# Kernel optimization log

Measured on AMD Instinct MI355X. Metric: run time of the kernel, lower is better.

## Reference

```python
import jax, jax.numpy as jnp
import numpy as np

N_NODES = 200000
N_GRAPHS = 64
K_SLOTS = 16
LATENT = 128
HID = 128  # hidden_dim // 2


def setup_inputs() -> dict:
    key = jax.random.key(0)
    ks = jax.random.split(key, 8)
    z = jax.random.normal(ks[0], (N_GRAPHS, K_SLOTS, LATENT), dtype=jnp.float32)
    s = jax.random.uniform(ks[1], (N_NODES, K_SLOTS), dtype=jnp.float32)
    batch = jnp.sort(jax.random.randint(ks[2], (N_NODES,), 0, N_GRAPHS))
    sc1 = 1.0 / np.sqrt(LATENT)
    sc2 = 1.0 / np.sqrt(HID)
    W1 = jax.random.normal(ks[3], (LATENT, HID), dtype=jnp.float32) * sc1
    b1 = jnp.zeros((HID,), dtype=jnp.float32)
    W2 = jax.random.normal(ks[4], (HID, HID), dtype=jnp.float32) * sc2
    b2 = jnp.zeros((HID,), dtype=jnp.float32)
    Wp = jax.random.normal(ks[5], (HID, 2), dtype=jnp.float32) * sc2
    bp = jnp.zeros((2,), dtype=jnp.float32)
    Wv = jax.random.normal(ks[6], (HID, 2), dtype=jnp.float32) * sc2
    bv = jnp.zeros((2,), dtype=jnp.float32)
    return {"z": z, "s": s, "batch": batch, "W1": W1, "b1": b1,
            "W2": W2, "b2": b2, "Wp": Wp, "bp": bp, "Wv": Wv, "bv": bv}


def reference(z, s, batch, W1, b1, W2, b2, Wp, bp, Wv, bv):
    # gather per-node latent set: [N, K, D]
    z_expanded = z[batch]
    # weighted sum over K slots -> [N, D]
    node_feat = jnp.einsum('nk,nkd->nd', s, z_expanded)
    # shared MLP: Linear-ReLU-Linear-ReLU
    h = jax.nn.relu(node_feat @ W1 + b1)
    h = jax.nn.relu(h @ W2 + b2)
    # heads
    pos_recon = jnp.tanh(h @ Wp + bp)
    vel_recon = h @ Wv + bv
    return jnp.concatenate([pos_recon, vel_recon], axis=-1)
```

## Files before the change

kernel.cpp:

```cpp
#include <hip/hip_runtime.h>

typedef _Float16 half4 __attribute__((ext_vector_type(4)));
typedef _Float16 half8 __attribute__((ext_vector_type(8)));
typedef float    f32x4 __attribute__((ext_vector_type(4)));

#define MFMA16(a,b,c) __builtin_amdgcn_mfma_f32_16x16x16f16((a),(b),(c),0,0,0)
#define MFMA32(a,b,c) __builtin_amdgcn_mfma_f32_16x16x32_f16((a),(b),(c),0,0,0)

static constexpr int N_NODES  = 200000;
static constexpr int N_GRAPHS = 64;
static constexpr int SGPG     = 128;
static constexpr int TOTAL_SG = N_GRAPHS * SGPG;

static constexpr size_t WS_ZWT    = 0;
static constexpr size_t WS_W2T    = 262144;
static constexpr size_t WS_WHT    = 294912;
static constexpr size_t WS_GSTART = 299008;


__global__ __launch_bounds__(256) void gnn_prep(
    const int* __restrict__ batch,
    const float* __restrict__ z,
    const float* __restrict__ W1,
    const float* __restrict__ W2,
    const float* __restrict__ Wp,
    const float* __restrict__ Wv,
    int* __restrict__ gstart,
    _Float16* __restrict__ zwt,
    _Float16* __restrict__ w2t,
    _Float16* __restrict__ wht)
{
    const int b = blockIdx.x, t = threadIdx.x;
    if (b < 782) {
        const int i = b * 256 + t;
        if (i < N_NODES) {
            const int bi   = batch[i];
            const int prev = (i == 0) ? -1 : batch[i - 1];
            if (bi != prev)
                for (int g = prev + 1; g <= bi; ++g) gstart[g] = i;
            if (i == N_NODES - 1)
                for (int g = bi + 1; g <= N_GRAPHS; ++g) gstart[g] = N_NODES;
        }
    } else if (b < 846) {
        const int e = (b - 782) * 256 + t;
        const int n = e >> 7, kk = e & 127;
        w2t[e] = (_Float16)W2[kk * 128 + n];
    } else if (b < 854) {
        const int e = (b - 846) * 256 + t;
        const int j = e >> 7, d = e & 127;
        float v = 0.f;
        if (j < 2)      v = Wp[d * 2 + j];
        else if (j < 4) v = Wv[d * 2 + (j - 2)];
        wht[e] = (_Float16)v;
    } else {
        const int p = (b - 854) * 2 + (t >> 7);
        const int g = p >> 4, k = p & 15, d = t & 127;
        const float* zr = z + (g * 16 + k) * 128;
        float a0 = 0.f, a1 = 0.f, a2 = 0.f, a3 = 0.f;
#pragma unroll 8
        for (int c = 0; c < 128; c += 4) {
            a0 += zr[c    ] * W1[(c    ) * 128 + d];
            a1 += zr[c + 1] * W1[(c + 1) * 128 + d];
            a2 += zr[c + 2] * W1[(c + 2) * 128 + d];
            a3 += zr[c + 3] * W1[(c + 3) * 128 + d];
        }
        zwt[(g * 128 + d) * 16 + k] = (_Float16)((a0 + a1) + (a2 + a3));
    }
}

__device__ inline float fast_tanh(float x) {
    x = fminf(fmaxf(x, -15.f), 15.f);
    const float e = __expf(2.f * x);
    return (e - 1.f) / (e + 1.f);
}

__device__ __forceinline__ half4 cvt4(f32x4 v) {
    half4 r;
    r[0] = (_Float16)v[0]; r[1] = (_Float16)v[1];
    r[2] = (_Float16)v[2]; r[3] = (_Float16)v[3];
    return r;
}

__device__ __forceinline__ void load_s(const float* __restrict__ s,
                                       int base, int ge, int n16, int quad,
                                       f32x4& a, f32x4& b)
{
    const f32x4 z4 = {0.f, 0.f, 0.f, 0.f};
    a = z4; b = z4;
    if (base + n16 < ge)      a = *(const f32x4*)(s + (base + n16) * 16 + quad * 4);
    if (base + 16 + n16 < ge) b = *(const f32x4*)(s + (base + 16 + n16) * 16 + quad * 4);
}

__device__ __forceinline__ void compute_sg(
    int g, int base, int ge,
    half4 bsA, half4 bsB,
    const _Float16* __restrict__ zwt,
    const half8* a2l, const half4* a3l,
    const float* b1l, const float* b2l,
    f32x4 c3init, float* __restrict__ out,
    int lane, int n16, int quad)
{
    const int nodeA = base + n16;
    const int nodeB = base + 16 + n16;
    const bool vA = nodeA < ge;
    const bool vB = nodeB < ge;

    const _Float16* zg = zwt + g * 2048;
    half8 h1a8[4], h1b8[4];
#pragma unroll
    for (int mt = 0; mt < 8; ++mt) {
        const half4 a1 = *(const half4*)(zg + (mt * 16 + n16) * 16 + quad * 4);
        const f32x4 cb = *(const f32x4*)(b1l + mt * 16 + quad * 4);
        const f32x4 accA = MFMA16(a1, bsA, cb);
        const f32x4 accB = MFMA16(a1, bsB, cb);
        const int tp  = mt >> 1;
        const int off = (mt & 1) * 4;
#pragma unroll
        for (int i = 0; i < 4; ++i) {
            h1a8[tp][off + i] = (_Float16)fmaxf(accA[i], 0.f);
            h1b8[tp][off + i] = (_Float16)fmaxf(accB[i], 0.f);
        }
    }

    f32x4 acc3a = c3init, acc3b = c3init;
    __builtin_amdgcn_s_setprio(1);
#pragma unroll
    for (int mo = 0; mo < 8; ++mo) {
        const f32x4 cb = *(const f32x4*)(b2l + mo * 16 + quad * 4);
        f32x4 a2a = cb, a2b = cb;
#pragma unroll
        for (int tp = 0; tp < 4; ++tp) {
            const half8 w = a2l[(mo * 4 + tp) * 64 + lane];
            a2a = MFMA32(w, h1a8[tp], a2a);
            a2b = MFMA32(w, h1b8[tp], a2b);
        }
        half4 h2a, h2b;
#pragma unroll
        for (int i = 0; i < 4; ++i) {
            h2a[i] = (_Float16)fmaxf(a2a[i], 0.f);
            h2b[i] = (_Float16)fmaxf(a2b[i], 0.f);
        }
        const half4 w3 = a3l[mo * 64 + lane];
        acc3a = MFMA16(w3, h2a, acc3a);
        acc3b = MFMA16(w3, h2b, acc3b);
    }
    __builtin_amdgcn_s_setprio(0);

    if (quad == 0) {
        if (vA) {
            f32x4 o;
            o[0] = fast_tanh(acc3a[0]); o[1] = fast_tanh(acc3a[1]);
            o[2] = acc3a[2];            o[3] = acc3a[3];
            *(f32x4*)(out + nodeA * 4) = o;
        }
        if (vB) {
            f32x4 o;
            o[0] = fast_tanh(acc3b[0]); o[1] = fast_tanh(acc3b[1]);
            o[2] = acc3b[2];            o[3] = acc3b[3];
            *(f32x4*)(out + nodeB * 4) = o;
        }
    }
}

__global__ __launch_bounds__(256, 4) void gnn_main(
    const float* __restrict__ s,
    const float* __restrict__ b1,
    const float* __restrict__ b2,
    const float* __restrict__ bp,
    const float* __restrict__ bv,
    const _Float16* __restrict__ zwt,
    const _Float16* __restrict__ w2t,
    const _Float16* __restrict__ wht,
    const int* __restrict__ gstart,
    float* __restrict__ out)
{
    __shared__ char lds[37888];
    half8* a2l = (half8*)lds;
    half4* a3l = (half4*)(lds + 32768);
    float* b1l = (float*)(lds + 36864);
    float* b2l = (float*)(lds + 37376);

    const int tid  = threadIdx.x;
    const int lane = tid & 63;
    const int n16  = lane & 15;
    const int quad = lane >> 4;

#pragma unroll
    for (int r = 0; r < 8; ++r) {
        const int e  = r * 256 + tid;
        const int mo = e >> 8, tp = (e >> 6) & 3, ll = e & 63;
        const int nn = ll & 15, qq = ll >> 4;
        const _Float16* srcp = w2t + (mo * 16 + nn) * 128 + tp * 32 + qq * 4;
        half8 v;
        *(half4*)&v     = *(const half4*)srcp;
        *((half4*)&v+1) = *(const half4*)(srcp + 16);
        a2l[e] = v;
    }
    {
        const int e = tid;
#pragma unroll
        for (int r = 0; r < 2; ++r) {
            const int ee = r * 256 + e;
            const int tt = ee >> 6, ll = ee & 63;
            const int nn = ll & 15, qq = ll >> 4;
            a3l[ee] = *(const half4*)(wht + nn * 128 + tt * 16 + qq * 4);
        }
        if (tid < 128)      b1l[tid] = b1[tid];
        else                b2l[tid - 128] = b2[tid - 128];
    }
    __syncthreads();

    const float bp0 = bp[0], bp1 = bp[1], bv0 = bv[0], bv1 = bv[1];
    f32x4 c3init = {0.f, 0.f, 0.f, 0.f};
    if (quad == 0) { c3init[0] = bp0; c3init[1] = bp1; c3init[2] = bv0; c3init[3] = bv1; }

    const int wid = blockIdx.x * 4 + (tid >> 6);
    const int nw  = gridDim.x * 4;

    const int sg0 = wid;
    const int sg1 = wid + nw;

    const int g0 = sg0 >> 7;
    const int gs0 = gstart[g0], ge0 = gstart[g0 + 1];
    const int base0 = gs0 + (sg0 & 127) * 32;
    const bool act0 = base0 < ge0;

    const bool in1 = sg1 < TOTAL_SG;
    const int g1 = in1 ? (sg1 >> 7) : 0;
    const int gs1 = in1 ? gstart[g1] : 0;
    const int ge1 = in1 ? gstart[g1 + 1] : 0;
    const int base1 = gs1 + (sg1 & 127) * 32;
    const bool act1 = in1 && (base1 < ge1);

    f32x4 sA0, sB0, sA1, sB1;
    const f32x4 z4 = {0.f, 0.f, 0.f, 0.f};
    sA0 = z4; sB0 = z4; sA1 = z4; sB1 = z4;
    if (act0) load_s(s, base0, ge0, n16, quad, sA0, sB0);
    if (act1) load_s(s, base1, ge1, n16, quad, sA1, sB1);

    if (act0) {
        compute_sg(g0, base0, ge0, cvt4(sA0), cvt4(sB0),
                   zwt, a2l, a3l, b1l, b2l, c3init, out, lane, n16, quad);
    }
    if (act1) {
        compute_sg(g1, base1, ge1, cvt4(sA1), cvt4(sB1),
                   zwt, a2l, a3l, b1l, b2l, c3init, out, lane, n16, quad);
    }

    for (int sgi = wid + 2 * nw; sgi < TOTAL_SG; sgi += nw) {
        const int g    = sgi >> 7;
        const int gs   = gstart[g];
        const int ge   = gstart[g + 1];
        const int base = gs + (sgi & 127) * 32;
        if (base >= ge) continue;
        f32x4 sa, sb;
        load_s(s, base, ge, n16, quad, sa, sb);
        compute_sg(g, base, ge, cvt4(sa), cvt4(sb),
                   zwt, a2l, a3l, b1l, b2l, c3init, out, lane, n16, quad);
    }
}

extern "C" void kernel_launch(void* const* d_in, const int* in_sizes, int n_in,
                              void* d_out, int out_size, void* d_ws, size_t ws_size,
                              hipStream_t stream)
{
    const float* z     = (const float*)d_in[0];
    const float* s     = (const float*)d_in[1];
    const int*   batch = (const int*)d_in[2];
    const float* W1    = (const float*)d_in[3];
    const float* b1    = (const float*)d_in[4];
    const float* W2    = (const float*)d_in[5];
    const float* b2    = (const float*)d_in[6];
    const float* Wp    = (const float*)d_in[7];
    const float* bp    = (const float*)d_in[8];
    const float* Wv    = (const float*)d_in[9];
    const float* bv    = (const float*)d_in[10];
    float* out = (float*)d_out;

    char* w = (char*)d_ws;
    _Float16* zwt = (_Float16*)(w + WS_ZWT);
    _Float16* w2t = (_Float16*)(w + WS_W2T);
    _Float16* wht = (_Float16*)(w + WS_WHT);
    int* gstart   = (int*)(w + WS_GSTART);

    hipLaunchKernelGGL(gnn_prep, dim3(1366), dim3(256), 0, stream,
                       batch, z, W1, W2, Wp, Wv, gstart, zwt, w2t, wht);
    hipLaunchKernelGGL(gnn_main, dim3(1024), dim3(256), 0, stream,
                       s, b1, b2, bp, bv, zwt, w2t, wht, gstart, out);
}
```

Before: 111.1 us.

## Convert W2/head weights in main kernel and interleave two subgraphs per wave

Removes the W2 and head-weight transpose/convert work from the prep kernel; the main kernel now reads the fp32 weights directly and converts them while filling LDS. The first two subgraphs of each wave are computed together, with four independent MFMA chains interleaved, so matrix-unit latency is hidden better. The setprio hint moves from the per-subgraph routine to the fused block. In exchange each of the 1024 blocks does strided fp32 gathers of W2 (redundant global traffic), and the interleaved block uses more registers.

```diff
diff --git a/kernel.cpp b/kernel.cpp
--- a/kernel.cpp
+++ b/kernel.cpp
@@ -13,22 +13,14 @@
 static constexpr int TOTAL_SG = N_GRAPHS * SGPG;
 
 static constexpr size_t WS_ZWT    = 0;
-static constexpr size_t WS_W2T    = 262144;
-static constexpr size_t WS_WHT    = 294912;
-static constexpr size_t WS_GSTART = 299008;
-
+static constexpr size_t WS_GSTART = 262144;
 
 __global__ __launch_bounds__(256) void gnn_prep(
     const int* __restrict__ batch,
     const float* __restrict__ z,
     const float* __restrict__ W1,
-    const float* __restrict__ W2,
-    const float* __restrict__ Wp,
-    const float* __restrict__ Wv,
     int* __restrict__ gstart,
-    _Float16* __restrict__ zwt,
-    _Float16* __restrict__ w2t,
-    _Float16* __restrict__ wht)
+    _Float16* __restrict__ zwt)
 {
     const int b = blockIdx.x, t = threadIdx.x;
     if (b < 782) {
@@ -41,19 +33,8 @@
             if (i == N_NODES - 1)
                 for (int g = bi + 1; g <= N_GRAPHS; ++g) gstart[g] = N_NODES;
         }
-    } else if (b < 846) {
-        const int e = (b - 782) * 256 + t;
-        const int n = e >> 7, kk = e & 127;
-        w2t[e] = (_Float16)W2[kk * 128 + n];
-    } else if (b < 854) {
-        const int e = (b - 846) * 256 + t;
-        const int j = e >> 7, d = e & 127;
-        float v = 0.f;
-        if (j < 2)      v = Wp[d * 2 + j];
-        else if (j < 4) v = Wv[d * 2 + (j - 2)];
-        wht[e] = (_Float16)v;
     } else {
-        const int p = (b - 854) * 2 + (t >> 7);
+        const int p = (b - 782) * 2 + (t >> 7);
         const int g = p >> 4, k = p & 15, d = t & 127;
         const float* zr = z + (g * 16 + k) * 128;
         float a0 = 0.f, a1 = 0.f, a2 = 0.f, a3 = 0.f;
@@ -123,7 +104,6 @@
     }
 
     f32x4 acc3a = c3init, acc3b = c3init;
-    __builtin_amdgcn_s_setprio(1);
 #pragma unroll
     for (int mo = 0; mo < 8; ++mo) {
         const f32x4 cb = *(const f32x4*)(b2l + mo * 16 + quad * 4);
@@ -144,7 +124,6 @@
         acc3a = MFMA16(w3, h2a, acc3a);
         acc3b = MFMA16(w3, h2b, acc3b);
     }
-    __builtin_amdgcn_s_setprio(0);
 
     if (quad == 0) {
         if (vA) {
@@ -169,8 +148,9 @@
     const float* __restrict__ bp,
     const float* __restrict__ bv,
     const _Float16* __restrict__ zwt,
-    const _Float16* __restrict__ w2t,
-    const _Float16* __restrict__ wht,
+    const float* __restrict__ W2,
+    const float* __restrict__ Wp,
+    const float* __restrict__ Wv,
     const int* __restrict__ gstart,
     float* __restrict__ out)
 {
@@ -190,20 +170,31 @@
         const int e  = r * 256 + tid;
         const int mo = e >> 8, tp = (e >> 6) & 3, ll = e & 63;
         const int nn = ll & 15, qq = ll >> 4;
-        const _Float16* srcp = w2t + (mo * 16 + nn) * 128 + tp * 32 + qq * 4;
+        const int dcol = mo * 16 + nn;
+        const int c0   = tp * 32 + qq * 4;
         half8 v;
-        *(half4*)&v     = *(const half4*)srcp;
-        *((half4*)&v+1) = *(const half4*)(srcp + 16);
+#pragma unroll
+        for (int j = 0; j < 4; ++j) v[j]     = (_Float16)W2[(c0 + j) * 128 + dcol];
+#pragma unroll
+        for (int j = 0; j < 4; ++j) v[4 + j] = (_Float16)W2[(c0 + 16 + j) * 128 + dcol];
         a2l[e] = v;
     }
     {
-        const int e = tid;
 #pragma unroll
         for (int r = 0; r < 2; ++r) {
-            const int ee = r * 256 + e;
+            const int ee = r * 256 + tid;
             const int tt = ee >> 6, ll = ee & 63;
             const int nn = ll & 15, qq = ll >> 4;
-            a3l[ee] = *(const half4*)(wht + nn * 128 + tt * 16 + qq * 4);
+            half4 v;
+#pragma unroll
+            for (int i = 0; i < 4; ++i) {
+                const int d = tt * 16 + qq * 4 + i;
+                float x = 0.f;
+                if (nn < 2)      x = Wp[d * 2 + nn];
+                else if (nn < 4) x = Wv[d * 2 + (nn - 2)];
+                v[i] = (_Float16)x;
+            }
+            a3l[ee] = v;
         }
         if (tid < 128)      b1l[tid] = b1[tid];
         else                b2l[tid - 128] = b2[tid - 128];
@@ -220,13 +211,13 @@
     const int sg0 = wid;
     const int sg1 = wid + nw;
 
-    const int g0 = sg0 >> 7;
+    const int g0  = sg0 >> 7;
     const int gs0 = gstart[g0], ge0 = gstart[g0 + 1];
     const int base0 = gs0 + (sg0 & 127) * 32;
     const bool act0 = base0 < ge0;
 
     const bool in1 = sg1 < TOTAL_SG;
-    const int g1 = in1 ? (sg1 >> 7) : 0;
+    const int g1  = in1 ? (sg1 >> 7) : 0;
     const int gs1 = in1 ? gstart[g1] : 0;
     const int ge1 = in1 ? gstart[g1 + 1] : 0;
     const int base1 = gs1 + (sg1 & 127) * 32;
@@ -238,13 +229,90 @@
     if (act0) load_s(s, base0, ge0, n16, quad, sA0, sB0);
     if (act1) load_s(s, base1, ge1, n16, quad, sA1, sB1);
 
-    if (act0) {
-        compute_sg(g0, base0, ge0, cvt4(sA0), cvt4(sB0),
-                   zwt, a2l, a3l, b1l, b2l, c3init, out, lane, n16, quad);
-    }
-    if (act1) {
-        compute_sg(g1, base1, ge1, cvt4(sA1), cvt4(sB1),
-                   zwt, a2l, a3l, b1l, b2l, c3init, out, lane, n16, quad);
+    if (act0 || act1) {
+        const half4 bs0A = cvt4(sA0), bs0B = cvt4(sB0);
+        const half4 bs1A = cvt4(sA1), bs1B = cvt4(sB1);
+        const _Float16* zg0 = zwt + g0 * 2048;
+        const _Float16* zg1 = zwt + g1 * 2048;
+
+        half8 h10a[4], h10b[4], h11a[4], h11b[4];
+#pragma unroll
+        for (int mt = 0; mt < 8; ++mt) {
+            const half4 a10 = *(const half4*)(zg0 + (mt * 16 + n16) * 16 + quad * 4);
+            const half4 a11 = *(const half4*)(zg1 + (mt * 16 + n16) * 16 + quad * 4);
+            const f32x4 cb  = *(const f32x4*)(b1l + mt * 16 + quad * 4);
+            const f32x4 acc0A = MFMA16(a10, bs0A, cb);
+            const f32x4 acc0B = MFMA16(a10, bs0B, cb);
+            const f32x4 acc1A = MFMA16(a11, bs1A, cb);
+            const f32x4 acc1B = MFMA16(a11, bs1B, cb);
+            const int tp  = mt >> 1;
+            const int off = (mt & 1) * 4;
+#pragma unroll
+            for (int i = 0; i < 4; ++i) {
+                h10a[tp][off + i] = (_Float16)fmaxf(acc0A[i], 0.f);
+                h10b[tp][off + i] = (_Float16)fmaxf(acc0B[i], 0.f);
+                h11a[tp][off + i] = (_Float16)fmaxf(acc1A[i], 0.f);
+                h11b[tp][off + i] = (_Float16)fmaxf(acc1B[i], 0.f);
+            }
+        }
+
+        f32x4 acc3_0a = c3init, acc3_0b = c3init;
+        f32x4 acc3_1a = c3init, acc3_1b = c3init;
+        __builtin_amdgcn_s_setprio(1);
+#pragma unroll
+        for (int mo = 0; mo < 8; ++mo) {
+            const f32x4 cb = *(const f32x4*)(b2l + mo * 16 + quad * 4);
+            f32x4 a0a = cb, a0b = cb, a1a = cb, a1b = cb;
+#pragma unroll
+            for (int tp = 0; tp < 4; ++tp) {
+                const half8 w = a2l[(mo * 4 + tp) * 64 + lane];
+                a0a = MFMA32(w, h10a[tp], a0a);
+                a0b = MFMA32(w, h10b[tp], a0b);
+                a1a = MFMA32(w, h11a[tp], a1a);
+                a1b = MFMA32(w, h11b[tp], a1b);
+            }
+            half4 h20a, h20b, h21a, h21b;
+#pragma unroll
+            for (int i = 0; i < 4; ++i) {
+                h20a[i] = (_Float16)fmaxf(a0a[i], 0.f);
+                h20b[i] = (_Float16)fmaxf(a0b[i], 0.f);
+                h21a[i] = (_Float16)fmaxf(a1a[i], 0.f);
+                h21b[i] = (_Float16)fmaxf(a1b[i], 0.f);
+            }
+            const half4 w3 = a3l[mo * 64 + lane];
+            acc3_0a = MFMA16(w3, h20a, acc3_0a);
+            acc3_0b = MFMA16(w3, h20b, acc3_0b);
+            acc3_1a = MFMA16(w3, h21a, acc3_1a);
+            acc3_1b = MFMA16(w3, h21b, acc3_1b);
+        }
+        __builtin_amdgcn_s_setprio(0);
+
+        if (quad == 0) {
+            if (act0 && (base0 + n16 < ge0)) {
+                f32x4 o;
+                o[0] = fast_tanh(acc3_0a[0]); o[1] = fast_tanh(acc3_0a[1]);
+                o[2] = acc3_0a[2];            o[3] = acc3_0a[3];
+                *(f32x4*)(out + (base0 + n16) * 4) = o;
+            }
+            if (act0 && (base0 + 16 + n16 < ge0)) {
+                f32x4 o;
+                o[0] = fast_tanh(acc3_0b[0]); o[1] = fast_tanh(acc3_0b[1]);
+                o[2] = acc3_0b[2];            o[3] = acc3_0b[3];
+                *(f32x4*)(out + (base0 + 16 + n16) * 4) = o;
+            }
+            if (act1 && (base1 + n16 < ge1)) {
+                f32x4 o;
+                o[0] = fast_tanh(acc3_1a[0]); o[1] = fast_tanh(acc3_1a[1]);
+                o[2] = acc3_1a[2];            o[3] = acc3_1a[3];
+                *(f32x4*)(out + (base1 + n16) * 4) = o;
+            }
+            if (act1 && (base1 + 16 + n16 < ge1)) {
+                f32x4 o;
+                o[0] = fast_tanh(acc3_1b[0]); o[1] = fast_tanh(acc3_1b[1]);
+                o[2] = acc3_1b[2];            o[3] = acc3_1b[3];
+                *(f32x4*)(out + (base1 + 16 + n16) * 4) = o;
+            }
+        }
     }
 
     for (int sgi = wid + 2 * nw; sgi < TOTAL_SG; sgi += nw) {
@@ -279,12 +347,10 @@
 
     char* w = (char*)d_ws;
     _Float16* zwt = (_Float16*)(w + WS_ZWT);
-    _Float16* w2t = (_Float16*)(w + WS_W2T);
-    _Float16* wht = (_Float16*)(w + WS_WHT);
     int* gstart   = (int*)(w + WS_GSTART);
 
-    hipLaunchKernelGGL(gnn_prep, dim3(1366), dim3(256), 0, stream,
-                       batch, z, W1, W2, Wp, Wv, gstart, zwt, w2t, wht);
+    hipLaunchKernelGGL(gnn_prep, dim3(1294), dim3(256), 0, stream,
+                       batch, z, W1, gstart, zwt);
     hipLaunchKernelGGL(gnn_main, dim3(1024), dim3(256), 0, stream,
-                       s, b1, b2, bp, bv, zwt, w2t, wht, gstart, out);
-}
+                       s, b1, b2, bp, bv, zwt, W2, Wp, Wv, gstart, out);
+}
```

Result: faster. 106.4 us (-4.3%).
